# Kernel tuning notes

Measured on AMD Instinct MI355X. Metric: run time of the kernel, lower is better.

The kernel has to match this reference:

```python
import jax, jax.numpy as jnp
import numpy as np

B, S, HID, NH, D = 8, 1024, 768, 12, 64
LENGTHS = np.array([1024, 896, 768, 640, 1024, 512, 768, 896], dtype=np.int64)


def setup_inputs() -> dict:
    key = jax.random.key(0)
    k1, k2 = jax.random.split(key)
    total = int(LENGTHS.sum())  # 6528

    cu_seqlens = jnp.asarray(np.concatenate([[0], np.cumsum(LENGTHS)]), dtype=jnp.int32)
    # flattened (b*s) positions of valid tokens, per flash-attn bert_padding
    indices = jnp.asarray(
        np.concatenate([b * S + np.arange(L) for b, L in enumerate(LENGTHS)]),
        dtype=jnp.int64)
    # 0 = valid token, 1 = pad (original checks attn_mask == 0 for valid)
    attn_mask = jnp.asarray(
        (np.arange(S)[None, :] >= LENGTHS[:, None]).astype(np.int32))

    hidden_states = jax.random.normal(k1, (total, HID), dtype=jnp.float32) * 0.02
    Wqkv_w = jax.random.normal(k2, (3 * HID, HID), dtype=jnp.float32) * 0.02
    Wqkv_b = jnp.zeros((3 * HID,), dtype=jnp.float32)

    # ALiBi bias fused with padding mask, as mosaic passes alibi_attn_mask
    slopes = 2.0 ** (-8.0 * np.arange(1, NH + 1) / NH)  # (NH,)
    pos = np.arange(S)
    rel = -np.abs(pos[None, :] - pos[:, None]).astype(np.float32)  # (S,S)
    alibi_hss = slopes[:, None, None].astype(np.float32) * rel      # (NH,S,S)
    pad_bias = np.where(np.asarray(attn_mask)[:, None, None, :] == 0, 0.0, -10000.0)
    alibi = jnp.asarray(alibi_hss[None] + pad_bias, dtype=jnp.float32)  # (B,NH,S,S)

    return {
        "hidden_states": hidden_states,
        "Wqkv_w": Wqkv_w,
        "Wqkv_b": Wqkv_b,
        "alibi": alibi,
        "cu_seqlens": cu_seqlens,
        "max_seqlen_in_batch": S,
        "indices": indices,
        "attn_mask": attn_mask,
    }


def reference(hidden_states, Wqkv_w, Wqkv_b, alibi, cu_seqlens,
              max_seqlen_in_batch, indices, attn_mask):
    batch = cu_seqlens.shape[0] - 1
    s = max_seqlen_in_batch
    nh = alibi.shape[1]
    d = hidden_states.shape[1] // nh

    # packed QKV projection on unpadded tokens: (nnz, 3*hid)
    qkv = hidden_states @ Wqkv_w.T + Wqkv_b
    # pad_input: scatter into (b*s, 3*hid), then view (b, s, 3, h, d)
    qkv_pad = jnp.zeros((batch * s, qkv.shape[-1]), dtype=qkv.dtype).at[indices].set(qkv)
    qkv_pad = qkv_pad.reshape(batch, s, 3, nh, d)
    q, k, v = qkv_pad[:, :, 0], qkv_pad[:, :, 1], qkv_pad[:, :, 2]  # (b, s, h, d)

    scale = 1.0 / jnp.sqrt(jnp.asarray(d, dtype=q.dtype))
    scores = jnp.einsum('bshd,bthd->bhst', q, k) * scale + alibi  # (b, h, s, s)
    probs = jax.nn.softmax(scores, axis=-1)
    ctx = jnp.einsum('bhst,bthd->bshd', probs, v)  # (b, s, h, d)

    # unpad_input: gather valid tokens back to (nnz, h*d)
    ctx = ctx.reshape(batch * s, nh * d)[indices]
    return ctx
```

## Files before the change

### kernel.cpp

```cpp
#include <hip/hip_runtime.h>
#include <hip/hip_bf16.h>
#include <stdint.h>


typedef __attribute__((ext_vector_type(8))) __bf16 bf16x8;
typedef __attribute__((ext_vector_type(8))) short short8;
typedef __attribute__((ext_vector_type(4))) short short4v;
typedef __attribute__((ext_vector_type(4))) float f32x4;
typedef __attribute__((ext_vector_type(2))) unsigned int u32x2;
typedef unsigned int u32;

#define AS1 __attribute__((address_space(1)))
#define AS3 __attribute__((address_space(3)))

static __device__ __forceinline__ unsigned short f2bf(float x) {
  unsigned u = __builtin_bit_cast(unsigned, x);
  u += 0x7fffu + ((u >> 16) & 1u);
  return (unsigned short)(u >> 16);
}
static __device__ __forceinline__ bf16x8 ld8s(const short* p) {
  return __builtin_bit_cast(bf16x8, *(const short8*)p);
}
static __device__ __forceinline__ u32 cvtpk(float lo, float hi) {
  u32 r;
  asm("v_cvt_pk_bf16_f32 %0, %1, %2" : "=v"(r) : "v"(lo), "v"(hi));
  return r;
}
static __device__ __forceinline__ f32x4 mfma16(u32x2 a, u32x2 b, f32x4 c) {
  asm("v_mfma_f32_16x16x16_bf16 %0, %1, %2, %0" : "+v"(c) : "v"(a), "v"(b));
  return c;
}
static __device__ __forceinline__ float vexp2(float x) {
  float r;
  asm("v_exp_f32 %0, %1" : "=v"(r) : "v"(x));
  return r;
}

__device__ const float g_slope[12] = {
  0.6299605249f, 0.3968502630f, 0.25f,          0.1574901312f,
  0.0992125657f, 0.0625f,       0.0393725328f,  0.0248031414f,
  0.015625f,     0.0098431332f, 0.0062007854f,  0.00390625f
};

__global__ __launch_bounds__(256) void convert_in(
    const float* __restrict__ hidden, const float* __restrict__ W,
    short* __restrict__ hb, short* __restrict__ wb)
{
  constexpr int NA = 6528 * 768;
  constexpr int NW = 2304 * 768;
  const int tot4 = (NA + NW) / 4;
  for (int idx = blockIdx.x * 256 + threadIdx.x; idx < tot4; idx += gridDim.x * 256) {
    const int e0 = idx * 4;
    const float* src; short* dst; int off;
    if (e0 < NA) { src = hidden; dst = hb; off = e0; }
    else         { src = W;      dst = wb; off = e0 - NA; }
    f32x4 v = *((const f32x4*)(src + off));
    short4v o;
    o[0] = (short)f2bf(v[0]); o[1] = (short)f2bf(v[1]);
    o[2] = (short)f2bf(v[2]); o[3] = (short)f2bf(v[3]);
    *(short4v*)(dst + off) = o;
  }
}

__global__ __launch_bounds__(256, 2) void qkv_gemm(
    const short* __restrict__ A, const short* __restrict__ W,
    const float* __restrict__ bias,
    short* __restrict__ qws, short* __restrict__ kws, short* __restrict__ vtws)
{
  constexpr int CUb[9] = {0,1024,1920,2688,3328,4352,4864,5632,6528};
  __shared__ __align__(16) short As[256 * 32];
  __shared__ __align__(16) short Bs[128 * 32];
  const int tid  = threadIdx.x;
  const int lane = tid & 63, w = tid >> 6;
  const int g = lane >> 4, c = lane & 15;
  const int wm = w >> 1, wn = w & 1;
  const int bm = blockIdx.x, bn = blockIdx.y;

  const short* Ab = A + (size_t)bm * 256 * 768;
  const short* Wb = W + (size_t)bn * 128 * 768;

  f32x4 acc[8][4] = {};
  const int sR = lane >> 2;
  const int sC = (lane & 3) ^ (sR & 3);

  for (int kt = 0; kt < 24; ++kt) {
    if (kt) __syncthreads();
#pragma unroll
    for (int i = 0; i < 4; ++i) {
      const int j = w * 4 + i;
      const AS1 unsigned int* ga =
        (const AS1 unsigned int*)(Ab + (size_t)(j * 16 + sR) * 768 + kt * 32 + sC * 8);
      __builtin_amdgcn_global_load_lds(ga, (AS3 unsigned int*)&As[j * 512], 16, 0, 0);
    }
#pragma unroll
    for (int i = 0; i < 2; ++i) {
      const int j = w * 2 + i;
      const AS1 unsigned int* gb =
        (const AS1 unsigned int*)(Wb + (size_t)(j * 16 + sR) * 768 + kt * 32 + sC * 8);
      __builtin_amdgcn_global_load_lds(gb, (AS3 unsigned int*)&Bs[j * 512], 16, 0, 0);
    }
    __syncthreads();

    const int xg = (g ^ (c & 3)) << 3;
    bf16x8 bfr[4];
#pragma unroll
    for (int nt = 0; nt < 4; ++nt)
      bfr[nt] = ld8s(&Bs[(wn * 64 + nt * 16 + c) * 32 + xg]);
#pragma unroll
    for (int mt = 0; mt < 8; ++mt) {
      bf16x8 af = ld8s(&As[(wm * 128 + mt * 16 + c) * 32 + xg]);
#pragma unroll
      for (int nt = 0; nt < 4; ++nt)
        acc[mt][nt] = __builtin_amdgcn_mfma_f32_16x16x32_bf16(af, bfr[nt], acc[mt][nt], 0, 0, 0);
    }
  }

  const int row0 = bm * 256 + wm * 128;
  if (row0 >= 6528) return;
  int b = 0;
#pragma unroll
  for (int i = 0; i < 8; ++i) if (row0 >= CUb[i + 1]) b = i + 1;
  const int col0  = bn * 128 + wn * 64;
  const int which = col0 / 768;
  const int hh    = (col0 % 768) / 64;
  const int srow0 = row0 - CUb[b];

  float bb[4];
#pragma unroll
  for (int nt = 0; nt < 4; ++nt) bb[nt] = bias[col0 + nt * 16 + c];

  if (which < 2) {
    const float sc = which ? 1.0f : 0.18033688011112042f;
    short* dst = (which ? kws : qws) + (size_t)(b * 12 + hh) * 1024 * 64;
#pragma unroll
    for (int mt = 0; mt < 8; ++mt)
#pragma unroll
      for (int nt = 0; nt < 4; ++nt)
#pragma unroll
        for (int r = 0; r < 4; ++r) {
          const int s = srow0 + mt * 16 + g * 4 + r;
          dst[(size_t)s * 64 + nt * 16 + c] = (short)f2bf((acc[mt][nt][r] + bb[nt]) * sc);
        }
  } else {
    short* dst = vtws + (size_t)(b * 12 + hh) * 64 * 1024;
#pragma unroll
    for (int mt = 0; mt < 8; ++mt)
#pragma unroll
      for (int nt = 0; nt < 4; ++nt) {
        const int s = srow0 + mt * 16 + g * 4;
        short4v pk;
        pk[0] = (short)f2bf(acc[mt][nt][0] + bb[nt]);
        pk[1] = (short)f2bf(acc[mt][nt][1] + bb[nt]);
        pk[2] = (short)f2bf(acc[mt][nt][2] + bb[nt]);
        pk[3] = (short)f2bf(acc[mt][nt][3] + bb[nt]);
        *(short4v*)&dst[(size_t)(nt * 16 + c) * 1024 + s] = pk;
      }
  }
}

__global__ __launch_bounds__(256, 2) void attn(
    const short* __restrict__ qws, const short* __restrict__ kws,
    const short* __restrict__ vtws, float* __restrict__ out)
{
  constexpr int CU[9]  = {0,1024,1920,2688,3328,4352,4864,5632,6528};
  constexpr int CQT[9] = {0,8,15,21,26,34,38,44,51};
  __shared__ __align__(16) short Ks[2][64 * 64];
  __shared__ __align__(16) short Vs[2][64 * 64];
  const int tid = threadIdx.x, lane = tid & 63, w = tid >> 6;
  const int g = lane >> 4, c = lane & 15;
  const int h = blockIdx.y;
  const int gq = blockIdx.x;
  int b = 0;
#pragma unroll
  for (int i = 0; i < 8; ++i) if (gq >= CQT[i + 1]) b = i + 1;
  const int qt = gq - CQT[b];
  const int Lb = CU[b + 1] - CU[b];
  const int sb = qt * 128 + w * 32;
  const size_t bh = (size_t)(b * 12 + h) * 1024 * 64;
  const short* qp = qws + bh;
  const short* kp = kws + bh;
  const short* vp = vtws + bh;
  const float slope2 = g_slope[h] * 1.4426950408889634f;

  const int sRow = lane >> 3;
  const int sChk = (lane & 7) ^ (sRow & 7);

  bf16x8 qf[2][2];
#pragma unroll
  for (int qh = 0; qh < 2; ++qh)
#pragma unroll
    for (int ks = 0; ks < 2; ++ks)
      qf[qh][ks] = ld8s(qp + (size_t)(sb + qh * 16 + c) * 64 + ks * 32 + g * 8);

  float srowf[2];
#pragma unroll
  for (int qh = 0; qh < 2; ++qh) srowf[qh] = (float)(sb + qh * 16 + c);

  f32x4 accO[2][4] = {};
  float l_part[2] = {};

  auto kaddr = [&](int row, int chunk) { return row * 64 + ((chunk ^ (row & 7)) << 3); };
  auto vaddr = [&](int row, int nt) {
    return row * 64 + (((2 * nt + (g >> 1)) ^ (row & 7)) << 3) + ((g & 1) << 2);
  };

#pragma unroll
  for (int i = 0; i < 2; ++i) {
    const int j = w * 2 + i;
    const int row = j * 8 + sRow;
    const AS1 unsigned int* gk =
      (const AS1 unsigned int*)(kp + (size_t)row * 64 + sChk * 8);
    __builtin_amdgcn_global_load_lds(gk, (AS3 unsigned int*)&Ks[0][j * 512], 16, 0, 0);
    const AS1 unsigned int* gv =
      (const AS1 unsigned int*)(vp + (size_t)row * 1024 + sChk * 8);
    __builtin_amdgcn_global_load_lds(gv, (AS3 unsigned int*)&Vs[0][j * 512], 16, 0, 0);
  }
  __syncthreads();

  int cur = 0;
  for (int t0 = 0; t0 < Lb; t0 += 64) {
    if (t0 + 64 < Lb) {
#pragma unroll
      for (int i = 0; i < 2; ++i) {
        const int j = w * 2 + i;
        const int row = j * 8 + sRow;
        const AS1 unsigned int* gk =
          (const AS1 unsigned int*)(kp + (size_t)(t0 + 64 + row) * 64 + sChk * 8);
        __builtin_amdgcn_global_load_lds(gk, (AS3 unsigned int*)&Ks[cur ^ 1][j * 512], 16, 0, 0);
        const AS1 unsigned int* gv =
          (const AS1 unsigned int*)(vp + (size_t)row * 1024 + (t0 + 64) + sChk * 8);
        __builtin_amdgcn_global_load_lds(gv, (AS3 unsigned int*)&Vs[cur ^ 1][j * 512], 16, 0, 0);
      }
    }

    f32x4 sa[2][4];
    __builtin_amdgcn_s_setprio(1);
#pragma unroll
    for (int nt = 0; nt < 4; ++nt) {
      bf16x8 kf0 = ld8s(&Ks[cur][kaddr(nt * 16 + c, g)]);
      bf16x8 kf1 = ld8s(&Ks[cur][kaddr(nt * 16 + c, 4 + g)]);
#pragma unroll
      for (int qh = 0; qh < 2; ++qh) {
        f32x4 z = {};
        z = __builtin_amdgcn_mfma_f32_16x16x32_bf16(kf0, qf[qh][0], z, 0, 0, 0);
        sa[qh][nt] = __builtin_amdgcn_mfma_f32_16x16x32_bf16(kf1, qf[qh][1], z, 0, 0, 0);
      }
    }
    __builtin_amdgcn_s_setprio(0);

    u32x2 pa[2][4];
    const float tg = (float)(t0 + g * 4);
#pragma unroll
    for (int qh = 0; qh < 2; ++qh) {
#pragma unroll
      for (int nt = 0; nt < 4; ++nt) {
        float p[4];
#pragma unroll
        for (int r = 0; r < 4; ++r) {
          const float d = srowf[qh] - (tg + (float)(nt * 16 + r));
          p[r] = vexp2(fmaf(-slope2, fabsf(d), sa[qh][nt][r]));
          l_part[qh] += p[r];
        }
        pa[qh][nt][0] = cvtpk(p[0], p[1]);
        pa[qh][nt][1] = cvtpk(p[2], p[3]);
      }
    }

    __builtin_amdgcn_s_setprio(1);
#pragma unroll
    for (int ntd = 0; ntd < 4; ++ntd) {
#pragma unroll
      for (int nt = 0; nt < 4; ++nt) {
        u32x2 vb = *(const u32x2*)&Vs[cur][vaddr(c + 16 * ntd, nt)];
        accO[0][ntd] = mfma16(pa[0][nt], vb, accO[0][ntd]);
        accO[1][ntd] = mfma16(pa[1][nt], vb, accO[1][ntd]);
      }
    }
    __builtin_amdgcn_s_setprio(0);

    __syncthreads();
    cur ^= 1;
  }

  float linv[2][4];
#pragma unroll
  for (int qh = 0; qh < 2; ++qh) {
    float rs = l_part[qh];
    rs += __shfl_xor(rs, 16, 64);
    rs += __shfl_xor(rs, 32, 64);
    const float inv = 1.0f / rs;
#pragma unroll
    for (int r = 0; r < 4; ++r)
      linv[qh][r] = __shfl(inv, g * 4 + r, 64);
  }

#pragma unroll
  for (int qh = 0; qh < 2; ++qh)
#pragma unroll
    for (int r = 0; r < 4; ++r) {
      const int srow = sb + qh * 16 + g * 4 + r;
      const size_t ob = (size_t)(CU[b] + srow) * 768 + h * 64;
#pragma unroll
      for (int ntd = 0; ntd < 4; ++ntd)
        out[ob + ntd * 16 + c] = accO[qh][ntd][r] * linv[qh][r];
    }
}

extern "C" void kernel_launch(void* const* d_in, const int* in_sizes, int n_in,
                              void* d_out, int out_size, void* d_ws, size_t ws_size,
                              hipStream_t stream) {
  const float* hidden = (const float*)d_in[0];
  const float* Wqkv_w = (const float*)d_in[1];
  const float* Wqkv_b = (const float*)d_in[2];

  constexpr size_t NA_PAD = (size_t)6656 * 768;
  constexpr size_t NW = (size_t)2304 * 768;
  constexpr size_t NP = (size_t)8 * 12 * 1024 * 64;

  short* hb   = (short*)d_ws;
  short* wb   = hb + NA_PAD;
  short* qws  = wb + NW;
  short* kws  = qws + NP;
  short* vtws = kws + NP;

  convert_in<<<dim3(2048), 256, 0, stream>>>(hidden, Wqkv_w, hb, wb);
  qkv_gemm<<<dim3(26, 18), 256, 0, stream>>>(hb, wb, Wqkv_b, qws, kws, vtws);
  attn<<<dim3(51, 12), 256, 0, stream>>>(qws, kws, vtws, (float*)d_out);
}
```

Before: 85.40 us.

## Triple-buffer QKV GEMM shared-memory tiles with async prefetch two steps ahead

The QKV projection GEMM now keeps three LDS buffers for its A and W tiles. It issues global-to-LDS loads for k-step kt+2 while computing on step kt, using explicit vmcnt waits and a single barrier per step in place of two syncthreads. The aim is to hide global memory latency behind MFMA work and cut barrier overhead. In exchange, shared memory per block triples, which can limit occupancy, and correctness now depends on the hand-written waitcnt accounting.

```diff
diff --git a/kernel.cpp b/kernel.cpp
--- a/kernel.cpp
+++ b/kernel.cpp
@@ -68,8 +68,8 @@
     short* __restrict__ qws, short* __restrict__ kws, short* __restrict__ vtws)
 {
   constexpr int CUb[9] = {0,1024,1920,2688,3328,4352,4864,5632,6528};
-  __shared__ __align__(16) short As[256 * 32];
-  __shared__ __align__(16) short Bs[128 * 32];
+  __shared__ __align__(16) short As[3][256 * 32];
+  __shared__ __align__(16) short Bs[3][128 * 32];
   const int tid  = threadIdx.x;
   const int lane = tid & 63, w = tid >> 6;
   const int g = lane >> 4, c = lane & 15;
@@ -82,37 +82,53 @@
   f32x4 acc[8][4] = {};
   const int sR = lane >> 2;
   const int sC = (lane & 3) ^ (sR & 3);
-
-  for (int kt = 0; kt < 24; ++kt) {
-    if (kt) __syncthreads();
+  const int xg = (g ^ (c & 3)) << 3;
+
+  auto stage = [&](int kt, short* bufA, short* bufB) {
 #pragma unroll
     for (int i = 0; i < 4; ++i) {
       const int j = w * 4 + i;
       const AS1 unsigned int* ga =
         (const AS1 unsigned int*)(Ab + (size_t)(j * 16 + sR) * 768 + kt * 32 + sC * 8);
-      __builtin_amdgcn_global_load_lds(ga, (AS3 unsigned int*)&As[j * 512], 16, 0, 0);
+      __builtin_amdgcn_global_load_lds(ga, (AS3 unsigned int*)&bufA[j * 512], 16, 0, 0);
     }
 #pragma unroll
     for (int i = 0; i < 2; ++i) {
       const int j = w * 2 + i;
       const AS1 unsigned int* gb =
         (const AS1 unsigned int*)(Wb + (size_t)(j * 16 + sR) * 768 + kt * 32 + sC * 8);
-      __builtin_amdgcn_global_load_lds(gb, (AS3 unsigned int*)&Bs[j * 512], 16, 0, 0);
-    }
-    __syncthreads();
-
-    const int xg = (g ^ (c & 3)) << 3;
+      __builtin_amdgcn_global_load_lds(gb, (AS3 unsigned int*)&bufB[j * 512], 16, 0, 0);
+    }
+  };
+  auto compute = [&](const short* bufA, const short* bufB) {
     bf16x8 bfr[4];
 #pragma unroll
     for (int nt = 0; nt < 4; ++nt)
-      bfr[nt] = ld8s(&Bs[(wn * 64 + nt * 16 + c) * 32 + xg]);
+      bfr[nt] = ld8s(&bufB[(wn * 64 + nt * 16 + c) * 32 + xg]);
 #pragma unroll
     for (int mt = 0; mt < 8; ++mt) {
-      bf16x8 af = ld8s(&As[(wm * 128 + mt * 16 + c) * 32 + xg]);
+      bf16x8 af = ld8s(&bufA[(wm * 128 + mt * 16 + c) * 32 + xg]);
 #pragma unroll
       for (int nt = 0; nt < 4; ++nt)
         acc[mt][nt] = __builtin_amdgcn_mfma_f32_16x16x32_bf16(af, bfr[nt], acc[mt][nt], 0, 0, 0);
     }
+  };
+  auto step = [&](int kt, int bi) {
+    if (kt < 23) asm volatile("s_waitcnt vmcnt(6) lgkmcnt(0)" ::: "memory");
+    else         asm volatile("s_waitcnt vmcnt(0) lgkmcnt(0)" ::: "memory");
+    __builtin_amdgcn_s_barrier();
+    compute(As[bi], Bs[bi]);
+    if (kt + 2 < 24) stage(kt + 2, As[(bi + 2) % 3], Bs[(bi + 2) % 3]);
+  };
+
+  stage(0, As[0], Bs[0]);
+  stage(1, As[1], Bs[1]);
+
+#pragma unroll 1
+  for (int kt = 0; kt < 24; kt += 3) {
+    step(kt + 0, 0);
+    step(kt + 1, 1);
+    step(kt + 2, 2);
   }
 
   const int row0 = bm * 256 + wm * 128;
```

New measurement: 102.1 us. 1.2x slower.
